# Performance work log

Measured on AMD Instinct MI355X. Metric: run time of the kernel, lower is better.

Reference implementation:

```python
import jax, jax.numpy as jnp
import numpy as np

N_NODES = 100000


def _gcn_layer(h_in, W, b, src, dst, norm, num_nodes):
    # PyG GCNConv: linear transform first, then normalized scatter-add aggregation
    h = h_in @ W                                   # [N, out_dim]
    msg = h[src] * norm[:, None]                   # gather + scale over edges
    out = jax.ops.segment_sum(msg, dst, num_segments=num_nodes)
    return out + b


def setup_inputs() -> dict:
    key = jax.random.key(0)
    k1, k2, k3, k4, k5 = jax.random.split(key, 5)
    d_in, d_hid, d_out = 128, 128, 128
    x = jax.random.normal(k1, (N_NODES, d_in), dtype=jnp.float32)
    edge_index = jax.random.randint(k2, (2, 1600000), 0, N_NODES, dtype=jnp.int64)
    # Glorot-ish init for weights, zeros for bias (as in GCNConv defaults)
    W1 = jax.random.normal(k3, (d_in, d_hid), dtype=jnp.float32) / np.sqrt(d_in)
    b1 = jnp.zeros((d_hid,), dtype=jnp.float32)
    W2 = jax.random.normal(k4, (d_hid, d_out), dtype=jnp.float32) / np.sqrt(d_hid)
    b2 = jnp.zeros((d_out,), dtype=jnp.float32)
    return {"x": x, "edge_index": edge_index, "W1": W1, "b1": b1, "W2": W2, "b2": b2}


def reference(x, edge_index, W1, b1, W2, b2):
    num_nodes = x.shape[0]
    # Add self-loops (GCNConv default add_self_loops=True)
    loop = jnp.arange(num_nodes, dtype=edge_index.dtype)
    src = jnp.concatenate([edge_index[0], loop])
    dst = jnp.concatenate([edge_index[1], loop])
    # Symmetric normalization: deg^{-1/2}[src] * deg^{-1/2}[dst]
    deg = jax.ops.segment_sum(jnp.ones_like(dst, dtype=x.dtype), dst, num_segments=num_nodes)
    dinv = jnp.where(deg > 0, jax.lax.rsqrt(deg), 0.0)
    norm = dinv[src] * dinv[dst]                   # [E + N]

    h = _gcn_layer(x, W1, b1, src, dst, norm, num_nodes)
    h = jax.nn.relu(h)                             # dropout is identity in eval mode
    out = _gcn_layer(h, W2, b2, src, dst, norm, num_nodes)
    return out
```

## Files before the change

### kernel.cpp

```cpp
#include <hip/hip_runtime.h>


#define DIM 128
#define CAP 192
typedef unsigned short ushort_t;
typedef unsigned int uint_t;
typedef __attribute__((ext_vector_type(8))) short bf16x8;
typedef __attribute__((ext_vector_type(4))) float f32x4;
typedef __attribute__((ext_vector_type(2))) float f32x2;
typedef __attribute__((ext_vector_type(2))) unsigned int u32x2;

static __device__ __forceinline__ uint_t f2bf(float f) {
    union { float f; uint_t u; } c; c.f = f;
    uint_t u = c.u;
    return (u + 0x7FFFu + ((u >> 16) & 1u)) >> 16;
}
static __device__ __forceinline__ float bf2f(uint_t h) {
    union { uint_t u; float f; } c; c.u = h << 16;
    return c.f;
}
static __device__ __forceinline__ float as_f(uint_t u) {
    union { uint_t u; float f; } c; c.u = u;
    return c.f;
}
static __device__ __forceinline__ void gld16(const void* g, void* l) {
    __builtin_amdgcn_global_load_lds(
        (const __attribute__((address_space(1))) uint_t*)g,
        (__attribute__((address_space(3))) uint_t*)l, 16, 0, 0);
}

__global__ __launch_bounds__(256) void k_bin(const int* __restrict__ src,
                                             const int* __restrict__ dst,
                                             int* __restrict__ bcur,
                                             uint_t* __restrict__ stage,
                                             int E, int RB) {
    int e = blockIdx.x * 256 + threadIdx.x;
    if (e >= E) return;
    int slice = blockIdx.x & 31;
    int s = src[e], d = dst[e];
    int idx = slice * RB + (d >> 7);
    int c = atomicAdd(&bcur[idx], 1);
    if (c < CAP)
        stage[(size_t)idx * CAP + c] = (uint_t)((s << 7) | (d & 127));
}

__global__ __launch_bounds__(1024) void k_bscan(const int* __restrict__ bcur,
                                                int* __restrict__ bbase, int RB) {
    __shared__ int sdat[1024];
    int t = threadIdx.x;
    int v = 0;
    if (t < RB)
        #pragma unroll
        for (int s = 0; s < 32; ++s) v += min(bcur[s * RB + t], CAP);
    sdat[t] = v;
    __syncthreads();
    #pragma unroll
    for (int o = 1; o < 1024; o <<= 1) {
        int x = (t >= o) ? sdat[t - o] : 0;
        __syncthreads();
        sdat[t] += x;
        __syncthreads();
    }
    if (t < RB) bbase[t] = sdat[t] - v;
}

__global__ __launch_bounds__(256) void k_build(const uint_t* __restrict__ stage,
                                               const int* __restrict__ bcur,
                                               const int* __restrict__ bbase,
                                               int* __restrict__ off,
                                               float* __restrict__ dinv,
                                               int* __restrict__ csr_src,
                                               int RB, int N, int E) {
    __shared__ int scnt[33];
    __shared__ int cnt[128], excl[128], lcur[128];
    __shared__ uint_t ent[32 * CAP];
    int b = blockIdx.x, t = threadIdx.x;
    if (t < 32) scnt[t + 1] = min(bcur[t * RB + b], CAP);
    if (t == 0) scnt[0] = 0;
    if (t < 128) { cnt[t] = 0; lcur[t] = 0; }
    __syncthreads();
    if (t == 0)
        for (int s = 1; s <= 32; ++s) scnt[s] += scnt[s - 1];
    __syncthreads();
    int total = scnt[32];
    for (int s = 0; s < 32; ++s) {
        int c0 = scnt[s], c1 = scnt[s + 1];
        const uint_t* sp = stage + (size_t)(s * RB + b) * CAP - c0;
        for (int i = c0 + t; i < c1; i += 256) ent[i] = sp[i];
    }
    __syncthreads();
    for (int i = t; i < total; i += 256) atomicAdd(&cnt[ent[i] & 127], 1);
    __syncthreads();
    if (t < 128) excl[t] = cnt[t];
    __syncthreads();
    #pragma unroll
    for (int o = 1; o < 128; o <<= 1) {
        int x = 0;
        if (t < 128 && t >= o) x = excl[t - o];
        __syncthreads();
        if (t < 128) excl[t] += x;
        __syncthreads();
    }
    int base = bbase[b];
    if (t < 128) {
        excl[t] -= cnt[t];
        int node = (b << 7) + t;
        if (node < N) {
            off[node] = base + excl[t];
            dinv[node] = rsqrtf((float)cnt[t] + 1.0f);
        }
    }
    if (b == RB - 1 && t == 0) off[N] = E;
    __syncthreads();
    for (int i = t; i < total; i += 256) {
        uint_t v = ent[i];
        int dl = v & 127;
        int pos = base + excl[dl] + atomicAdd(&lcur[dl], 1);
        csr_src[pos] = (int)(v >> 7);
    }
}

__global__ __launch_bounds__(256) void k_prep(const float* __restrict__ W1,
                                              const float* __restrict__ W2,
                                              short* __restrict__ whi,
                                              short* __restrict__ wlo) {
    int g = blockIdx.x * 256 + threadIdx.x;
    int layer = g >> 11, c = g & 2047;
    const float* W = layer ? W2 : W1;
    int ks = c >> 9, nt = (c >> 6) & 7, l = c & 63;
    int q = l >> 4, m = l & 15;
    int n = nt * 16 + m;
    bf16x8 h8, l8;
    #pragma unroll
    for (int j = 0; j < 8; ++j) {
        int k = ks * 32 + q * 8 + j;
        float f = W[k * 128 + n];
        uint_t hb = f2bf(f);
        h8[j] = (short)hb;
        l8[j] = (short)f2bf(f - bf2f(hb));
    }
    ((bf16x8*)whi)[g] = h8;
    ((bf16x8*)wlo)[g] = l8;
}

template <int XMODE>
__global__ __launch_bounds__(256) void k_gemm(const short* __restrict__ afhi,
                                              const float* __restrict__ xsrc,
                                              const short* __restrict__ wfhi,
                                              const short* __restrict__ wflo,
                                              const float* __restrict__ dinv,
                                              ushort_t* __restrict__ hout, int M) {
    __shared__ short AH[8192], AL[8192], WH[8192], WL[8192];
    const int t = threadIdx.x;
    const int rb = blockIdx.x;
    const int wv = t >> 6, l = t & 63;
    const int mb = (wv & 1) * 4;
    const int nbc = (wv >> 1) * 4;

    f32x4 acc[4][4];
    #pragma unroll
    for (int i = 0; i < 4; ++i)
        #pragma unroll
        for (int j = 0; j < 4; ++j)
            acc[i][j] = (f32x4){0.f, 0.f, 0.f, 0.f};

    #pragma unroll
    for (int kc = 0; kc < 2; ++kc) {
        if (kc) __syncthreads();
        {
            const short* gh = wfhi + kc * 8192;
            const short* gl = wflo + kc * 8192;
            #pragma unroll
            for (int i = 0; i < 4; ++i) {
                int idx = (i * 256 + t) * 8;
                gld16(gh + idx, WH + idx);
                gld16(gl + idx, WL + idx);
            }
        }
        if (XMODE == 1) {
            const short* ga = afhi + (size_t)rb * 16384 + kc * 8192;
            #pragma unroll
            for (int i = 0; i < 4; ++i) {
                int idx = (i * 256 + t) * 8;
                gld16(ga + idx, AH + idx);
            }
        } else {
            #pragma unroll
            for (int i = 0; i < 4; ++i) {
                int cid = i * 256 + t;
                int row = cid >> 3, c7 = cid & 7;
                int node = rb * 128 + row;
                bf16x8 h8 = {}, l8 = {};
                if (node < M) {
                    const float* xp = xsrc + (size_t)node * 128 + kc * 64 + c7 * 8;
                    f32x4 fa = *(const f32x4*)xp;
                    f32x4 fb = *(const f32x4*)(xp + 4);
                    float f[8] = {fa[0], fa[1], fa[2], fa[3],
                                  fb[0], fb[1], fb[2], fb[3]};
                    #pragma unroll
                    for (int j = 0; j < 8; ++j) {
                        uint_t hb = f2bf(f[j]);
                        h8[j] = (short)hb;
                        l8[j] = (short)f2bf(f[j] - bf2f(hb));
                    }
                }
                int dstoff = row * 64 + ((c7 ^ (row & 7)) << 3);
                *(bf16x8*)&AH[dstoff] = h8;
                *(bf16x8*)&AL[dstoff] = l8;
            }
        }
        __syncthreads();
        #pragma unroll
        for (int ksl = 0; ksl < 2; ++ksl) {
            bf16x8 ah[4], al[4];
            #pragma unroll
            for (int i = 0; i < 4; ++i) {
                int rowl = (mb + i) * 16 + (l & 15);
                int cA = ksl * 4 + (l >> 4);
                int sa = rowl * 64 + ((cA ^ (rowl & 7)) << 3);
                ah[i] = *(const bf16x8*)&AH[sa];
                if (XMODE == 0) al[i] = *(const bf16x8*)&AL[sa];
            }
            #pragma unroll
            for (int j = 0; j < 4; ++j) {
                bf16x8 bh = *(const bf16x8*)&WH[((ksl * 8 + nbc + j) * 64 + l) * 8];
                bf16x8 bl = *(const bf16x8*)&WL[((ksl * 8 + nbc + j) * 64 + l) * 8];
                #pragma unroll
                for (int i = 0; i < 4; ++i) {
                    acc[i][j] = __builtin_amdgcn_mfma_f32_16x16x32_bf16(ah[i], bh, acc[i][j], 0, 0, 0);
                    if (XMODE == 0)
                        acc[i][j] = __builtin_amdgcn_mfma_f32_16x16x32_bf16(al[i], bh, acc[i][j], 0, 0, 0);
                    acc[i][j] = __builtin_amdgcn_mfma_f32_16x16x32_bf16(ah[i], bl, acc[i][j], 0, 0, 0);
                }
            }
        }
    }

    const int q = l >> 4, mm = l & 15;
    #pragma unroll
    for (int i = 0; i < 4; ++i)
        #pragma unroll
        for (int r = 0; r < 4; ++r) {
            int gr = rb * 128 + (wv & 1) * 64 + i * 16 + q * 4 + r;
            if (gr < M) {
                float di = dinv[gr];
                #pragma unroll
                for (int j = 0; j < 4; ++j)
                    hout[gr * 128 + nbc * 16 + j * 16 + mm] =
                        (ushort_t)f2bf(di * acc[i][j][r]);
            }
        }
}

template <int NB>
static __device__ __forceinline__ void gbatch(const int* __restrict__ csr,
                                              int e, int half,
                                              const u32x2* __restrict__ hrow,
                                              float& ax, float& ay,
                                              float& az, float& aw) {
    int s[NB]; u32x2 v[NB];
    #pragma unroll
    for (int u = 0; u < NB; ++u)
        s[u] = __builtin_nontemporal_load(&csr[e + 2 * u + half]);
    #pragma unroll
    for (int u = 0; u < NB; ++u) v[u] = hrow[(size_t)s[u] * 32];
    #pragma unroll
    for (int u = 0; u < NB; ++u) {
        ax += as_f(v[u].x << 16); ay += as_f(v[u].x & 0xffff0000u);
        az += as_f(v[u].y << 16); aw += as_f(v[u].y & 0xffff0000u);
    }
}

template <int FRAG>
__global__ __launch_bounds__(256) void k_agg(const uint_t* __restrict__ h32,
                                             const int* __restrict__ off,
                                             const int* __restrict__ csr_src,
                                             const float* __restrict__ dinv,
                                             const float* __restrict__ bias,
                                             float* __restrict__ out,
                                             uint_t* __restrict__ fhi, int N) {
    int n = (blockIdx.x * 256 + threadIdx.x) >> 6;
    if (n >= N) return;
    int l = threadIdx.x & 63;
    int half = l >> 5, c = l & 31;
    const u32x2* hrow = (const u32x2*)h32 + c;

    float ax = 0.f, ay = 0.f, az = 0.f, aw = 0.f;
    if (!half) {
        u32x2 sv = hrow[(size_t)n * 32];
        ax = as_f(sv.x << 16); ay = as_f(sv.x & 0xffff0000u);
        az = as_f(sv.y << 16); aw = as_f(sv.y & 0xffff0000u);
    }

    int e = off[n], end = off[n + 1];
    for (; e + 16 <= end; e += 16) gbatch<8>(csr_src, e, half, hrow, ax, ay, az, aw);
    if (e + 8 <= end) { gbatch<4>(csr_src, e, half, hrow, ax, ay, az, aw); e += 8; }
    if (e + 4 <= end) { gbatch<2>(csr_src, e, half, hrow, ax, ay, az, aw); e += 4; }
    if (e + 2 <= end) { gbatch<1>(csr_src, e, half, hrow, ax, ay, az, aw); e += 2; }
    if (e < end && !half) {
        int s = csr_src[e];
        u32x2 v = hrow[(size_t)s * 32];
        ax += as_f(v.x << 16); ay += as_f(v.x & 0xffff0000u);
        az += as_f(v.y << 16); aw += as_f(v.y & 0xffff0000u);
    }

    ax += __shfl_xor(ax, 32, 64);
    ay += __shfl_xor(ay, 32, 64);
    az += __shfl_xor(az, 32, 64);
    aw += __shfl_xor(aw, 32, 64);
    if (half) return;

    float di = dinv[n];
    f32x4 bv = *((const f32x4*)bias + c);
    ax = di * ax + bv[0];
    ay = di * ay + bv[1];
    az = di * az + bv[2];
    aw = di * aw + bv[3];

    if (FRAG) {
        ax = fmaxf(ax, 0.f); ay = fmaxf(ay, 0.f);
        az = fmaxf(az, 0.f); aw = fmaxf(aw, 0.f);
        uint_t w0h = (f2bf(ay) << 16) | f2bf(ax);
        uint_t w1h = (f2bf(aw) << 16) | f2bf(az);
        int rb = n >> 7, row = n & 127;
        int p7 = ((c >> 1) & 7) ^ (row & 7);
        size_t i2 = (size_t)rb * 4096 + (c >> 4) * 2048 + row * 16 + p7 * 2 + (c & 1);
        u32x2 vh; vh.x = w0h; vh.y = w1h;
        __builtin_nontemporal_store(vh, (u32x2*)fhi + i2);
    } else {
        f32x4 o; o[0] = ax; o[1] = ay; o[2] = az; o[3] = aw;
        __builtin_nontemporal_store(o, (f32x4*)out + (size_t)n * 32 + c);
    }
}

extern "C" void kernel_launch(void* const* d_in, const int* in_sizes, int n_in,
                              void* d_out, int out_size, void* d_ws, size_t ws_size,
                              hipStream_t stream) {
    const float* x  = (const float*)d_in[0];
    const int*   ei = (const int*)d_in[1];
    const float* W1 = (const float*)d_in[2];
    const float* b1 = (const float*)d_in[3];
    const float* W2 = (const float*)d_in[4];
    const float* b2 = (const float*)d_in[5];
    float* out = (float*)d_out;

    const int N = in_sizes[0] / DIM;
    const int E = in_sizes[1] / 2;
    const int* src = ei;
    const int* dst = ei + E;
    const int RB = (N + 127) / 128;

    char* w = (char*)d_ws;
    float* dinv    = (float*)(w);
    int*   bcur    = (int*)  (w + (1 << 19));
    int*   bbase   = (int*)  (w + (1 << 19) + (1 << 17));
    int*   off     = (int*)  (w + (3 << 19));
    short* whi     = (short*)(w + (1 << 21) + (1 << 13));
    short* wlo     = whi + 2 * 16384;
    int*   csr_src = (int*)  (w + ((size_t)5 << 19));
    short* fhi     = (short*)(w + ((size_t)17 << 20));
    ushort_t* hbuf = (ushort_t*)(w + ((size_t)69 << 20));
    uint_t* stage  = (uint_t*)hbuf;

    const int B = 256;
    const int agg_grid = (N * 64 + B - 1) / B;

    hipMemsetAsync(bcur, 0, (size_t)32 * RB * 4, stream);
    k_prep<<<16, B, 0, stream>>>(W1, W2, whi, wlo);
    k_bin<<<(E + B - 1) / B, B, 0, stream>>>(src, dst, bcur, stage, E, RB);
    k_bscan<<<1, 1024, 0, stream>>>(bcur, bbase, RB);
    k_build<<<RB, B, 0, stream>>>(stage, bcur, bbase, off, dinv, csr_src,
                                  RB, N, E);
    k_gemm<0><<<RB, B, 0, stream>>>(nullptr, x, whi, wlo, dinv, hbuf, N);
    k_agg<1><<<agg_grid, B, 0, stream>>>((const uint_t*)hbuf, off, csr_src,
                                         dinv, b1, nullptr,
                                         (uint_t*)fhi, N);
    k_gemm<1><<<RB, B, 0, stream>>>(fhi, nullptr, whi + 16384, wlo + 16384,
                                    dinv, hbuf, N);
    k_agg<0><<<agg_grid, B, 0, stream>>>((const uint_t*)hbuf, off, csr_src,
                                         dinv, b2, out,
                                         nullptr, N);
}
```

Measured before the change: 375.7 us.

## Drop bucket scan kernel using fixed-stride CSR buckets with per-node end offsets

Removes the single-block k_bscan prefix-scan launch. Each 128-node bucket now writes its CSR segment at a fixed stride (BSTRIDE) instead of a globally scanned base, and per-node end offsets are stored separately. Entries are first sorted in shared memory and then written out contiguously so the global stores are coalesced. This saves one serial kernel launch and one dependency in exchange for extra LDS in k_build and a CSR layout with gaps; buckets larger than BSTRIDE would silently drop edges.

```diff
diff --git a/kernel.cpp b/kernel.cpp
--- a/kernel.cpp
+++ b/kernel.cpp
@@ -3,6 +3,7 @@
 
 #define DIM 128
 #define CAP 192
+#define BSTRIDE 2816
 typedef unsigned short ushort_t;
 typedef unsigned int uint_t;
 typedef __attribute__((ext_vector_type(8))) short bf16x8;
@@ -44,36 +45,17 @@
         stage[(size_t)idx * CAP + c] = (uint_t)((s << 7) | (d & 127));
 }
 
-__global__ __launch_bounds__(1024) void k_bscan(const int* __restrict__ bcur,
-                                                int* __restrict__ bbase, int RB) {
-    __shared__ int sdat[1024];
-    int t = threadIdx.x;
-    int v = 0;
-    if (t < RB)
-        #pragma unroll
-        for (int s = 0; s < 32; ++s) v += min(bcur[s * RB + t], CAP);
-    sdat[t] = v;
-    __syncthreads();
-    #pragma unroll
-    for (int o = 1; o < 1024; o <<= 1) {
-        int x = (t >= o) ? sdat[t - o] : 0;
-        __syncthreads();
-        sdat[t] += x;
-        __syncthreads();
-    }
-    if (t < RB) bbase[t] = sdat[t] - v;
-}
-
 __global__ __launch_bounds__(256) void k_build(const uint_t* __restrict__ stage,
                                                const int* __restrict__ bcur,
-                                               const int* __restrict__ bbase,
                                                int* __restrict__ off,
+                                               int* __restrict__ nend,
                                                float* __restrict__ dinv,
                                                int* __restrict__ csr_src,
-                                               int RB, int N, int E) {
+                                               int RB, int N) {
     __shared__ int scnt[33];
     __shared__ int cnt[128], excl[128], lcur[128];
     __shared__ uint_t ent[32 * CAP];
+    __shared__ int sorted[BSTRIDE];
     int b = blockIdx.x, t = threadIdx.x;
     if (t < 32) scnt[t + 1] = min(bcur[t * RB + b], CAP);
     if (t == 0) scnt[0] = 0;
@@ -101,23 +83,26 @@
         if (t < 128) excl[t] += x;
         __syncthreads();
     }
-    int base = bbase[b];
+    int base = b * BSTRIDE;
     if (t < 128) {
         excl[t] -= cnt[t];
         int node = (b << 7) + t;
         if (node < N) {
-            off[node] = base + excl[t];
+            off[node]  = base + excl[t];
+            nend[node] = base + excl[t] + cnt[t];
             dinv[node] = rsqrtf((float)cnt[t] + 1.0f);
         }
     }
-    if (b == RB - 1 && t == 0) off[N] = E;
     __syncthreads();
     for (int i = t; i < total; i += 256) {
         uint_t v = ent[i];
         int dl = v & 127;
-        int pos = base + excl[dl] + atomicAdd(&lcur[dl], 1);
-        csr_src[pos] = (int)(v >> 7);
-    }
+        int pos = excl[dl] + atomicAdd(&lcur[dl], 1);
+        if (pos < BSTRIDE) sorted[pos] = (int)(v >> 7);
+    }
+    __syncthreads();
+    for (int i = t; i < total; i += 256)
+        csr_src[base + i] = sorted[i];
 }
 
 __global__ __launch_bounds__(256) void k_prep(const float* __restrict__ W1,
@@ -274,6 +259,7 @@
 template <int FRAG>
 __global__ __launch_bounds__(256) void k_agg(const uint_t* __restrict__ h32,
                                              const int* __restrict__ off,
+                                             const int* __restrict__ nend,
                                              const int* __restrict__ csr_src,
                                              const float* __restrict__ dinv,
                                              const float* __restrict__ bias,
@@ -292,7 +278,7 @@
         az = as_f(sv.y << 16); aw = as_f(sv.y & 0xffff0000u);
     }
 
-    int e = off[n], end = off[n + 1];
+    int e = off[n], end = nend[n];
     for (; e + 16 <= end; e += 16) gbatch<8>(csr_src, e, half, hrow, ax, ay, az, aw);
     if (e + 8 <= end) { gbatch<4>(csr_src, e, half, hrow, ax, ay, az, aw); e += 8; }
     if (e + 4 <= end) { gbatch<2>(csr_src, e, half, hrow, ax, ay, az, aw); e += 4; }
@@ -353,9 +339,9 @@
     char* w = (char*)d_ws;
     float* dinv    = (float*)(w);
     int*   bcur    = (int*)  (w + (1 << 19));
-    int*   bbase   = (int*)  (w + (1 << 19) + (1 << 17));
-    int*   off     = (int*)  (w + (3 << 19));
-    short* whi     = (short*)(w + (1 << 21) + (1 << 13));
+    int*   nend    = (int*)  (w + (1 << 19) + (1 << 17));
+    int*   off     = (int*)  (w + (1 << 20) + (1 << 17));
+    short* whi     = (short*)(w + (1 << 21) + (1 << 17));
     short* wlo     = whi + 2 * 16384;
     int*   csr_src = (int*)  (w + ((size_t)5 << 19));
     short* fhi     = (short*)(w + ((size_t)17 << 20));
@@ -368,16 +354,15 @@
     hipMemsetAsync(bcur, 0, (size_t)32 * RB * 4, stream);
     k_prep<<<16, B, 0, stream>>>(W1, W2, whi, wlo);
     k_bin<<<(E + B - 1) / B, B, 0, stream>>>(src, dst, bcur, stage, E, RB);
-    k_bscan<<<1, 1024, 0, stream>>>(bcur, bbase, RB);
-    k_build<<<RB, B, 0, stream>>>(stage, bcur, bbase, off, dinv, csr_src,
-                                  RB, N, E);
+    k_build<<<RB, B, 0, stream>>>(stage, bcur, off, nend, dinv, csr_src,
+                                  RB, N);
     k_gemm<0><<<RB, B, 0, stream>>>(nullptr, x, whi, wlo, dinv, hbuf, N);
-    k_agg<1><<<agg_grid, B, 0, stream>>>((const uint_t*)hbuf, off, csr_src,
+    k_agg<1><<<agg_grid, B, 0, stream>>>((const uint_t*)hbuf, off, nend, csr_src,
                                          dinv, b1, nullptr,
                                          (uint_t*)fhi, N);
     k_gemm<1><<<RB, B, 0, stream>>>(fhi, nullptr, whi + 16384, wlo + 16384,
                                     dinv, hbuf, N);
-    k_agg<0><<<agg_grid, B, 0, stream>>>((const uint_t*)hbuf, off, csr_src,
+    k_agg<0><<<agg_grid, B, 0, stream>>>((const uint_t*)hbuf, off, nend, csr_src,
                                          dinv, b2, out,
                                          nullptr, N);
 }
```

Result: faster. 368.2 us, median of 2 (-2.0%).
